# Kernel tuning notes

Hardware: AMD Instinct MI355X
Metric: run time of the kernel (lower is better)

The kernel has to match this reference:

```python
import jax, jax.numpy as jnp
import numpy as np

N = 50000
E = 400000
IN_DIM = 384
HID = 256
Q_DIM = 384
HEAD_HID = 128


def _glorot(key, shape):
    fan_in, fan_out = shape[0], shape[1]
    lim = float(np.sqrt(6.0 / (fan_in + fan_out)))
    return jax.random.uniform(key, shape, jnp.float32, -lim, lim)


def setup_inputs() -> dict:
    key = jax.random.key(0)
    ks = jax.random.split(key, 10)
    x = jax.random.normal(ks[0], (N, IN_DIM), jnp.float32)
    edge_index = jax.random.randint(ks[1], (2, E), 0, N, dtype=jnp.int64)
    q = jax.random.normal(ks[2], (Q_DIM,), jnp.float32)
    # layer 1: Linear(in_dim*2 + query_dim -> hidden)
    W1 = _glorot(ks[3], (IN_DIM * 2 + Q_DIM, HID))
    b1 = jnp.zeros((HID,), jnp.float32)
    # layer 2: Linear(hidden*2 + query_dim -> hidden)
    W2 = _glorot(ks[4], (HID * 2 + Q_DIM, HID))
    b2 = jnp.zeros((HID,), jnp.float32)
    # score head: Linear(hidden + query_dim -> 128) -> ReLU -> Linear(128 -> 1)
    Wh1 = _glorot(ks[5], (HID + Q_DIM, HEAD_HID))
    bh1 = jnp.zeros((HEAD_HID,), jnp.float32)
    Wh2 = _glorot(ks[6], (HEAD_HID, 1))
    bh2 = jnp.zeros((1,), jnp.float32)
    return {"x": x, "edge_index": edge_index, "q": q,
            "W1": W1, "b1": b1, "W2": W2, "b2": b2,
            "Wh1": Wh1, "bh1": bh1, "Wh2": Wh2, "bh2": bh2}


def _sage_layer(h, src, dst, q, W, b, n_nodes):
    # mean aggregation with self-loops: (sum_{j in N(i)} h_j + h_i) / (deg_i + 1)
    deg = jnp.zeros((n_nodes,), h.dtype).at[dst].add(1.0) + 1.0  # [N]
    agg = (jax.ops.segment_sum(h[src], dst, num_segments=n_nodes) + h) / deg[:, None]
    q_exp = jnp.broadcast_to(q, (n_nodes, q.shape[0]))
    cat = jnp.concatenate([h, agg, q_exp], axis=-1)  # [N, 2*d + q_dim]
    return jax.nn.relu(cat @ W + b)  # dropout is identity in eval mode


def reference(x, edge_index, q, W1, b1, W2, b2, Wh1, bh1, Wh2, bh2):
    src, dst = edge_index[0], edge_index[1]
    n = x.shape[0]
    h = _sage_layer(x, src, dst, q, W1, b1, n)
    h = _sage_layer(h, src, dst, q, W2, b2, n)
    q_exp = jnp.broadcast_to(q, (n, q.shape[0]))
    s = jax.nn.relu(jnp.concatenate([h, q_exp], axis=-1) @ Wh1 + bh1)
    logits = (s @ Wh2 + bh2).squeeze(-1)  # [N]
    return logits
```

## Files before the change

### kernel.cpp

```cpp
#include <hip/hip_runtime.h>
#include <cstdint>
#include <cstddef>

typedef unsigned short u16;
typedef short short8 __attribute__((ext_vector_type(8)));
typedef unsigned short u16x8 __attribute__((ext_vector_type(8)));
typedef unsigned short u16x4 __attribute__((ext_vector_type(4)));
typedef float f32x4 __attribute__((ext_vector_type(4)));

#define DEVI __device__ __forceinline__

#if defined(__has_builtin)
#if __has_builtin(__builtin_amdgcn_global_load_lds)
#define USE_GLD 1
#endif
#endif

DEVI float bf2f(u16 u) { return __uint_as_float(((unsigned)u) << 16); }
DEVI u16 f2bf(float f) {
  unsigned u = __float_as_uint(f);
  u += 0x7FFFu + ((u >> 16) & 1u);
  return (u16)(u >> 16);
}

DEVI void stage16(const u16* __restrict__ g, u16* lds_base, int lane) {
#ifdef USE_GLD
  __builtin_amdgcn_global_load_lds(
      (const __attribute__((address_space(1))) unsigned int*)g,
      (__attribute__((address_space(3))) unsigned int*)lds_base, 16, 0, 0);
#else
  *(u16x8*)(lds_base + lane * 8) = *(const u16x8*)g;
#endif
}

__global__ void build_deg(const int* __restrict__ dst, int* __restrict__ deg, int E) {
  int e = blockIdx.x * 256 + threadIdx.x;
  if (e < E) atomicAdd(&deg[dst[e]], 1);
}

__global__ __launch_bounds__(256) void scan1(const int* __restrict__ deg,
                                             int* __restrict__ pref,
                                             int* __restrict__ bsum, int Nn) {
  __shared__ int wsum[4];
  int i = blockIdx.x * 256 + threadIdx.x;
  int lane = threadIdx.x & 63, w = threadIdx.x >> 6;
  int v = (i < Nn) ? deg[i] : 0;
  int s = v;
  for (int off = 1; off < 64; off <<= 1) {
    int t = __shfl_up(s, off, 64);
    if (lane >= off) s += t;
  }
  if (lane == 63) wsum[w] = s;
  __syncthreads();
  int add = 0;
  for (int k = 0; k < w; ++k) add += wsum[k];
  int incl = s + add;
  if (i < Nn) pref[i] = incl - v;
  if (threadIdx.x == 255) bsum[blockIdx.x] = incl;
}

__global__ __launch_bounds__(256) void scan2(int* __restrict__ bsum,
                                             int* __restrict__ row_ofs,
                                             int nb, int Nn) {
  __shared__ int wsum[4];
  int t = threadIdx.x;
  int lane = t & 63, w = t >> 6;
  int v = (t < nb) ? bsum[t] : 0;
  int s = v;
  for (int off = 1; off < 64; off <<= 1) {
    int u = __shfl_up(s, off, 64);
    if (lane >= off) s += u;
  }
  if (lane == 63) wsum[w] = s;
  __syncthreads();
  int add = 0;
  for (int k = 0; k < w; ++k) add += wsum[k];
  int incl = s + add;
  if (t < nb) bsum[t] = incl - v;
  if (t == 255) row_ofs[Nn] = incl;
}

__global__ __launch_bounds__(256) void scan3(const int* __restrict__ pref,
                                             const int* __restrict__ bsum,
                                             int* __restrict__ row_ofs,
                                             int* __restrict__ cursor, int Nn) {
  int i = blockIdx.x * 256 + threadIdx.x;
  if (i < Nn) {
    int r = pref[i] + bsum[blockIdx.x];
    row_ofs[i] = r;
    cursor[i] = r;
  }
}

__global__ void csr_fill(const int* __restrict__ src, const int* __restrict__ dst,
                         int* __restrict__ cursor, int* __restrict__ col, int E) {
  int e = blockIdx.x * 256 + threadIdx.x;
  if (e < E) {
    int p = atomicAdd(&cursor[dst[e]], 1);
    col[p] = src[e];
  }
}

__global__ __launch_bounds__(256) void pack_all(
    const float* __restrict__ W1, const float* __restrict__ W2,
    const float* __restrict__ Wh1, u16* __restrict__ B1t,
    u16* __restrict__ B2t, u16* __restrict__ Bht) {
  int b = blockIdx.x;
  if (b < 1024) {
    int c = b >> 1;
    int k = (b & 1) * 256 + threadIdx.x;
    if (k < 384) {
      float v = (c < 256) ? W1[(size_t)k * 256 + c]
                          : W1[(size_t)(384 + k) * 256 + (c - 256)];
      B1t[(size_t)c * 384 + k] = f2bf(v);
    }
  } else if (b < 1536) {
    int c = b - 1024;
    int k = threadIdx.x;
    float v = (c < 256) ? W2[(size_t)k * 256 + c]
                        : W2[(size_t)(256 + k) * 256 + (c - 256)];
    B2t[(size_t)c * 256 + k] = f2bf(v);
  } else {
    int c = b - 1536;
    int k = threadIdx.x;
    Bht[(size_t)c * 256 + k] = f2bf(Wh1[(size_t)k * 128 + c]);
  }
}

__global__ __launch_bounds__(384) void bias_all(
    const float* __restrict__ W1, const float* __restrict__ b1,
    const float* __restrict__ W2, const float* __restrict__ b2,
    const float* __restrict__ Wh1, const float* __restrict__ bh1,
    const float* __restrict__ q, float* __restrict__ cq1,
    float* __restrict__ cq2, float* __restrict__ cqh) {
  __shared__ float part[6];
  int b = blockIdx.x;
  const float* W; const float* bb; float* o; int ld, roff, c;
  if (b < 256)      { W = W1;  bb = b1;  o = cq1; ld = 256; roff = 768; c = b; }
  else if (b < 512) { W = W2;  bb = b2;  o = cq2; ld = 256; roff = 512; c = b - 256; }
  else              { W = Wh1; bb = bh1; o = cqh; ld = 128; roff = 256; c = b - 512; }
  int t = threadIdx.x;
  float p = q[t] * W[(size_t)(roff + t) * ld + c];
  for (int off = 32; off > 0; off >>= 1) p += __shfl_down(p, off, 64);
  if ((t & 63) == 0) part[t >> 6] = p;
  __syncthreads();
  if (t == 0) {
    float acc = bb[c];
    for (int w = 0; w < 6; ++w) acc += part[w];
    o[c] = acc;
  }
}

#define W_NC 512
#define ES 520
#define OFF_A0 0
#define OFF_A1 (64 * 32)
#define OFF_B0 (2 * 64 * 32)
#define OFF_B1 (2 * 64 * 32 + 512 * 32)
#define SMEM_TOT (2 * 64 * 32 + 2 * 512 * 32)

#define GEMM512_COMPUTE(LA, LB)                                                \
  {                                                                            \
    short8 bfr[8];                                                             \
    _Pragma("unroll") for (int nt = 0; nt < 8; ++nt) bfr[nt] =                 \
        *(const short8*)&(LB)[((wave * 128 + nt * 16 + m) * 4 + csel) * 8];    \
    _Pragma("unroll") for (int mt = 0; mt < 4; ++mt) {                         \
      short8 af = *(const short8*)&(LA)[((mt * 16 + m) * 4 + csel) * 8];       \
      _Pragma("unroll") for (int nt = 0; nt < 8; ++nt)                         \
          acc[mt][nt] = __builtin_amdgcn_mfma_f32_16x16x32_bf16(               \
              af, bfr[nt], acc[mt][nt], 0, 0, 0);                              \
    }                                                                          \
  }

#define GEMM512_EPILOGUE()                                                     \
  {                                                                            \
    u16* et = lds_b0;                                                          \
    _Pragma("unroll") for (int mt = 0; mt < 4; ++mt) {                         \
      __syncthreads();                                                         \
      _Pragma("unroll") for (int nt = 0; nt < 8; ++nt) {                       \
        int col = wave * 128 + nt * 16 + m;                                    \
        float bb = (col < bias_len) ? bias[col] : 0.0f;                        \
        _Pragma("unroll") for (int r = 0; r < 4; ++r) {                        \
          float v = acc[mt][nt][r] + bb;                                       \
          if (relu) v = fmaxf(v, 0.0f);                                        \
          et[(quad * 4 + r) * ES + col] = f2bf(v);                             \
        }                                                                      \
      }                                                                        \
      __syncthreads();                                                         \
      _Pragma("unroll") for (int p = 0; p < 4; ++p) {                          \
        int row_loc = p * 4 + wave;                                            \
        int grow = row0 + mt * 16 + row_loc;                                   \
        if (grow < M)                                                          \
          *(u16x8*)&C[(size_t)grow * W_NC + lane * 8] =                        \
              *(const u16x8*)&et[row_loc * ES + lane * 8];                     \
      }                                                                        \
    }                                                                          \
  }

#define GEMM512_B_SETUP()                                                      \
  const u16* pbB[8];                                                           \
  _Pragma("unroll") for (int p = 0; p < 8; ++p) {                              \
    int L = p * 256 + tid;                                                     \
    int c = L >> 2, qs = L & 3;                                                \
    int g = qs ^ ((c >> 1) & 3);                                               \
    pbB[p] = Bt + (size_t)c * K + g * 8;                                       \
  }

#define GEMM512_B_STAGE2()                                                     \
  _Pragma("unroll") for (int p = 0; p < 8; ++p) {                              \
    u16* d = lds_b0 + (size_t)(p * 256 + wave * 64) * 8;                       \
    stage16(pbB[p], d, lane);                                                  \
    stage16(pbB[p] + 32, d + (512 * 32), lane);                                \
    pbB[p] += 64;                                                              \
  }

__global__ __launch_bounds__(256, 2) void gemm512_f32a(
    const float* __restrict__ A, const u16* __restrict__ Bt,
    u16* __restrict__ C, const float* __restrict__ bias,
    int M, int K, int bias_len, int relu) {
  __shared__ __align__(16) u16 smem[SMEM_TOT];
  u16* lds_a0 = smem + OFF_A0;
  u16* lds_a1 = smem + OFF_A1;
  u16* lds_b0 = smem + OFF_B0;
  u16* lds_b1 = smem + OFF_B1;

  const int tid = threadIdx.x;
  const int lane = tid & 63;
  const int wave = tid >> 6;
  const int row0 = blockIdx.x * 64;
  const int m = lane & 15;
  const int quad = lane >> 4;
  const int csel = quad ^ ((m >> 1) & 3);

  const int rA = tid >> 2;
  const int qA = tid & 3;
  const int sA = rA * 4 + (qA ^ ((rA >> 1) & 3));
  int ga = row0 + rA; if (ga >= M) ga = M - 1;
  const float* pa = A + (size_t)ga * K + qA * 8;

  GEMM512_B_SETUP()

  f32x4 acc[4][8] = {};

  f32x4 v0a = *(const f32x4*)pa, v0b = *(const f32x4*)(pa + 4);
  f32x4 v1a = *(const f32x4*)(pa + 32), v1b = *(const f32x4*)(pa + 36);
  pa += 64;

  for (int k0 = 0; k0 < K; k0 += 64) {
    __syncthreads();
    GEMM512_B_STAGE2()
    u16x8 h0, h1;
#pragma unroll
    for (int j = 0; j < 4; ++j) {
      h0[j] = f2bf(v0a[j]); h0[j + 4] = f2bf(v0b[j]);
      h1[j] = f2bf(v1a[j]); h1[j + 4] = f2bf(v1b[j]);
    }
    *(u16x8*)&lds_a0[sA * 8] = h0;
    *(u16x8*)&lds_a1[sA * 8] = h1;
    const float* pn = (k0 + 64 < K) ? pa : A;
    f32x4 n0a = *(const f32x4*)pn, n0b = *(const f32x4*)(pn + 4);
    f32x4 n1a = *(const f32x4*)(pn + 32), n1b = *(const f32x4*)(pn + 36);
    pa += 64;
    __syncthreads();
    GEMM512_COMPUTE(lds_a0, lds_b0)
    GEMM512_COMPUTE(lds_a1, lds_b1)
    v0a = n0a; v0b = n0b; v1a = n1a; v1b = n1b;
  }

  GEMM512_EPILOGUE()
}

__global__ __launch_bounds__(256, 2) void gemm512_bf16a(
    const u16* __restrict__ A, const u16* __restrict__ Bt,
    u16* __restrict__ C, const float* __restrict__ bias,
    int M, int K, int bias_len, int relu) {
  __shared__ __align__(16) u16 smem[SMEM_TOT];
  u16* lds_a0 = smem + OFF_A0;
  u16* lds_a1 = smem + OFF_A1;
  u16* lds_b0 = smem + OFF_B0;
  u16* lds_b1 = smem + OFF_B1;

  const int tid = threadIdx.x;
  const int lane = tid & 63;
  const int wave = tid >> 6;
  const int row0 = blockIdx.x * 64;
  const int m = lane & 15;
  const int quad = lane >> 4;
  const int csel = quad ^ ((m >> 1) & 3);

  const int rA = tid >> 2;
  const int qA = tid & 3;
  const int sA = rA * 4 + (qA ^ ((rA >> 1) & 3));
  int ga = row0 + rA; if (ga >= M) ga = M - 1;
  const u16* pa = A + (size_t)ga * K + qA * 8;

  GEMM512_B_SETUP()

  f32x4 acc[4][8] = {};

  u16x8 va0 = *(const u16x8*)pa;
  u16x8 va1 = *(const u16x8*)(pa + 32);
  pa += 64;

  for (int k0 = 0; k0 < K; k0 += 64) {
    __syncthreads();
    GEMM512_B_STAGE2()
    *(u16x8*)&lds_a0[sA * 8] = va0;
    *(u16x8*)&lds_a1[sA * 8] = va1;
    const u16* pn = (k0 + 64 < K) ? pa : A;
    u16x8 na0 = *(const u16x8*)pn;
    u16x8 na1 = *(const u16x8*)(pn + 32);
    pa += 64;
    __syncthreads();
    GEMM512_COMPUTE(lds_a0, lds_b0)
    GEMM512_COMPUTE(lds_a1, lds_b1)
    va0 = na0; va1 = na1;
  }

  GEMM512_EPILOGUE()
}

#define BM 128
#define BK 32

__global__ __launch_bounds__(256) void gemm_head(
    const u16* __restrict__ A, const u16* __restrict__ Bt,
    const float* __restrict__ cqh, const float* __restrict__ Wh2,
    const float* __restrict__ bh2, float* __restrict__ out, int M, int K) {
  __shared__ __align__(16) u16 lds_a[BM * BK];
  __shared__ __align__(16) u16 lds_b[BM * BK];
  __shared__ float red[128][2];

  const int tid = threadIdx.x;
  const int lane = tid & 63;
  const int wave = tid >> 6;
  const int wm = wave & 1, wn = wave >> 1;
  const int row0 = blockIdx.x * BM;
  const int m = lane & 15;
  const int quad = lane >> 4;
  const int csel = quad ^ ((m >> 1) & 3);

  const int r0 = tid >> 2, r1 = 64 + r0;
  const int cs = tid & 3;
  const int s0 = r0 * 4 + (cs ^ ((r0 >> 1) & 3));
  const int s1 = r1 * 4 + (cs ^ ((r1 >> 1) & 3));
  const int cb0 = cs ^ ((r0 >> 1) & 3);
  const int cb1 = cs ^ ((r1 >> 1) & 3);
  int ga0 = row0 + r0; if (ga0 >= M) ga0 = M - 1;
  int ga1 = row0 + r1; if (ga1 >= M) ga1 = M - 1;
  const u16* pa0 = A + (size_t)ga0 * K + cs * 8;
  const u16* pa1 = A + (size_t)ga1 * K + cs * 8;
  const u16* pb0 = Bt + (size_t)r0 * K + cb0 * 8;
  const u16* pb1 = Bt + (size_t)r1 * K + cb1 * 8;
  u16* lb0 = lds_b + (size_t)(wave * 64) * 8;
  u16* lb1 = lds_b + (size_t)(256 + wave * 64) * 8;

  f32x4 acc[4][4] = {};

  u16x8 va0 = *(const u16x8*)pa0; pa0 += BK;
  u16x8 va1 = *(const u16x8*)pa1; pa1 += BK;

  for (int k0 = 0; k0 < K; k0 += BK) {
    __syncthreads();
    stage16(pb0, lb0, lane); pb0 += BK;
    stage16(pb1, lb1, lane); pb1 += BK;
    *(u16x8*)&lds_a[s0 * 8] = va0;
    *(u16x8*)&lds_a[s1 * 8] = va1;
    const u16* n0 = (k0 + BK < K) ? pa0 : A;
    const u16* n1 = (k0 + BK < K) ? pa1 : A;
    u16x8 w0 = *(const u16x8*)n0;
    u16x8 w1 = *(const u16x8*)n1;
    pa0 += BK; pa1 += BK;
    __syncthreads();

    short8 af[4], bfv[4];
#pragma unroll
    for (int mt = 0; mt < 4; ++mt)
      af[mt] = *(const short8*)&lds_a[((wm * 64 + mt * 16 + m) * 4 + csel) * 8];
#pragma unroll
    for (int nt = 0; nt < 4; ++nt)
      bfv[nt] = *(const short8*)&lds_b[((wn * 64 + nt * 16 + m) * 4 + csel) * 8];
#pragma unroll
    for (int mt = 0; mt < 4; ++mt)
#pragma unroll
      for (int nt = 0; nt < 4; ++nt)
        acc[mt][nt] = __builtin_amdgcn_mfma_f32_16x16x32_bf16(
            af[mt], bfv[nt], acc[mt][nt], 0, 0, 0);
    va0 = w0; va1 = w1;
  }

  float part[4][4];
#pragma unroll
  for (int mt = 0; mt < 4; ++mt)
#pragma unroll
    for (int r = 0; r < 4; ++r) part[mt][r] = 0.0f;
#pragma unroll
  for (int nt = 0; nt < 4; ++nt) {
    int col = wn * 64 + nt * 16 + m;
    float bb = cqh[col];
    float w2 = Wh2[col];
#pragma unroll
    for (int mt = 0; mt < 4; ++mt)
#pragma unroll
      for (int r = 0; r < 4; ++r)
        part[mt][r] += fmaxf(acc[mt][nt][r] + bb, 0.0f) * w2;
  }
#pragma unroll
  for (int off = 8; off > 0; off >>= 1)
#pragma unroll
    for (int mt = 0; mt < 4; ++mt)
#pragma unroll
      for (int r = 0; r < 4; ++r)
        part[mt][r] += __shfl_xor(part[mt][r], off, 64);
  if (m == 0) {
#pragma unroll
    for (int mt = 0; mt < 4; ++mt)
#pragma unroll
      for (int r = 0; r < 4; ++r)
        red[wm * 64 + mt * 16 + quad * 4 + r][wn] = part[mt][r];
  }
  __syncthreads();
  if (tid < 128) {
    int grow = row0 + tid;
    if (grow < M) out[grow] = red[tid][0] + red[tid][1] + bh2[0];
  }
}

__global__ __launch_bounds__(256) void aggregate(
    const u16* __restrict__ C, const int* __restrict__ row_ofs,
    const int* __restrict__ col_idx, u16* __restrict__ H, int Nn) {
  int node = blockIdx.x * 8 + (threadIdx.x >> 5);
  if (node >= Nn) return;
  int l = threadIdx.x & 31;
  int s = row_ofs[node], e = row_ofs[node + 1];
  float inv = 1.0f / (float)(e - s + 1);
  const u16* crow = C + (size_t)node * 512;
  u16x8 y0 = *(const u16x8*)(crow + 256 + l * 8);
  float a[8];
#pragma unroll
  for (int j = 0; j < 8; ++j) a[j] = bf2f(y0[j]);
  int t = s;
  for (; t + 4 <= e; t += 4) {
    int j0 = col_idx[t], j1 = col_idx[t + 1], j2 = col_idx[t + 2], j3 = col_idx[t + 3];
    u16x8 v0 = *(const u16x8*)(C + (size_t)j0 * 512 + 256 + l * 8);
    u16x8 v1 = *(const u16x8*)(C + (size_t)j1 * 512 + 256 + l * 8);
    u16x8 v2 = *(const u16x8*)(C + (size_t)j2 * 512 + 256 + l * 8);
    u16x8 v3 = *(const u16x8*)(C + (size_t)j3 * 512 + 256 + l * 8);
#pragma unroll
    for (int j = 0; j < 8; ++j)
      a[j] += (bf2f(v0[j]) + bf2f(v1[j])) + (bf2f(v2[j]) + bf2f(v3[j]));
  }
  for (; t < e; ++t) {
    int jj = col_idx[t];
    u16x8 vj = *(const u16x8*)(C + (size_t)jj * 512 + 256 + l * 8);
#pragma unroll
    for (int j = 0; j < 8; ++j) a[j] += bf2f(vj[j]);
  }
  u16x8 u = *(const u16x8*)(crow + l * 8);
  u16x8 o;
#pragma unroll
  for (int j = 0; j < 8; ++j)
    o[j] = f2bf(fmaxf(bf2f(u[j]) + a[j] * inv, 0.0f));
  *(u16x8*)(H + (size_t)node * 256 + l * 8) = o;
}

extern "C" void kernel_launch(void* const* d_in, const int* in_sizes, int n_in,
                              void* d_out, int out_size, void* d_ws, size_t ws_size,
                              hipStream_t stream) {
  const float* x   = (const float*)d_in[0];
  const int*   ei  = (const int*)d_in[1];
  const float* q   = (const float*)d_in[2];
  const float* W1  = (const float*)d_in[3];
  const float* b1  = (const float*)d_in[4];
  const float* W2  = (const float*)d_in[5];
  const float* b2  = (const float*)d_in[6];
  const float* Wh1 = (const float*)d_in[7];
  const float* bh1 = (const float*)d_in[8];
  const float* Wh2 = (const float*)d_in[9];
  const float* bh2 = (const float*)d_in[10];

  const int N = in_sizes[0] / 384;
  const int E = in_sizes[1] / 2;
  const int Npad = ((N + 127) / 128) * 128;
  const int* esrc = ei;
  const int* edst = ei + E;

  size_t off = 0;
  auto alloc = [&](size_t bytes) -> void* {
    void* p = (char*)d_ws + off;
    off += (bytes + 255) & ~(size_t)255;
    return p;
  };
  int* deg     = (int*)alloc((size_t)N * 4);
  int* row_ofs = (int*)alloc((size_t)(N + 1) * 4);
  int* cursor  = (int*)alloc((size_t)N * 4);
  int* colidx  = (int*)alloc((size_t)E * 4);
  int* pref    = (int*)alloc((size_t)N * 4);
  int* bsum    = (int*)alloc(256 * 4);
  u16* B1t = (u16*)alloc((size_t)512 * 384 * 2);
  u16* B2t = (u16*)alloc((size_t)512 * 256 * 2);
  u16* Bht = (u16*)alloc((size_t)128 * 256 * 2);
  float* cq1 = (float*)alloc(256 * 4);
  float* cq2 = (float*)alloc(256 * 4);
  float* cqh = (float*)alloc(128 * 4);
  u16* Cbuf = (u16*)alloc((size_t)Npad * 512 * 2);
  u16* Hbuf = (u16*)alloc((size_t)Npad * 256 * 2);

  (void)hipMemsetAsync(deg, 0, (size_t)N * 4, stream);
  int eb = (E + 255) / 256;
  int nb = (N + 255) / 256;
  build_deg<<<eb, 256, 0, stream>>>(edst, deg, E);
  scan1<<<nb, 256, 0, stream>>>(deg, pref, bsum, N);
  scan2<<<1, 256, 0, stream>>>(bsum, row_ofs, nb, N);
  scan3<<<nb, 256, 0, stream>>>(pref, bsum, row_ofs, cursor, N);
  csr_fill<<<eb, 256, 0, stream>>>(esrc, edst, cursor, colidx, E);

  pack_all<<<1664, 256, 0, stream>>>(W1, W2, Wh1, B1t, B2t, Bht);
  bias_all<<<640, 384, 0, stream>>>(W1, b1, W2, b2, Wh1, bh1, q, cq1, cq2, cqh);

  int gb64 = (N + 63) / 64;
  int mb = Npad / 128;
  int nb8 = (N + 7) / 8;
  gemm512_f32a<<<gb64, 256, 0, stream>>>(x, B1t, Cbuf, cq1, N, 384, 256, 0);
  aggregate<<<nb8, 256, 0, stream>>>(Cbuf, row_ofs, colidx, Hbuf, N);
  gemm512_bf16a<<<gb64, 256, 0, stream>>>(Hbuf, B2t, Cbuf, cq2, N, 256, 256, 0);
  aggregate<<<nb8, 256, 0, stream>>>(Cbuf, row_ofs, colidx, Hbuf, N);
  gemm_head<<<mb, 256, 0, stream>>>(Hbuf, Bht, cqh, Wh2, bh2, (float*)d_out, N, 256);
}
```

Before: 339.6 us.

## Retile node GEMMs to 128x256 blocks with double-buffered LDS pipeline

Replaces the 64-row x 512-column GEMM blocks with 128-row x 256-column tiles, using 8 waves per block arranged 2x4, and splits the output columns across two blocks. The K loop now double-buffers A and B in LDS so that staging the next tile overlaps compute, leaving one barrier per iteration instead of two. This is meant to balance A/B reuse, cut accumulator registers per wave, and hide global-load latency. In exchange, the LDS footprint grows and the A tile is read twice, once per column half.

```diff
diff --git a/kernel.cpp b/kernel.cpp
--- a/kernel.cpp
+++ b/kernel.cpp
@@ -151,83 +151,87 @@
   }
 }
 
-#define W_NC 512
-#define ES 520
-#define OFF_A0 0
-#define OFF_A1 (64 * 32)
-#define OFF_B0 (2 * 64 * 32)
-#define OFF_B1 (2 * 64 * 32 + 512 * 32)
-#define SMEM_TOT (2 * 64 * 32 + 2 * 512 * 32)
-
-#define GEMM512_COMPUTE(LA, LB)                                                \
+#define G2_ACH 4096
+#define G2_ASZ 8192
+#define G2_BCH 8192
+#define G2_BSZ 16384
+#define G2_SMEM (2 * G2_ASZ + 2 * G2_BSZ)
+#define G2_ES 264
+
+#define G2_B_SETUP()                                                           \
+  const u16* pbB[2];                                                           \
+  _Pragma("unroll") for (int p = 0; p < 2; ++p) {                              \
+    int L = p * 512 + tid;                                                     \
+    int c = L >> 2, qs = L & 3;                                                \
+    int g = qs ^ ((c >> 1) & 3);                                               \
+    pbB[p] = Bt + (size_t)(cb * 256 + c) * K + g * 8;                          \
+  }
+
+#define G2_B_STAGE(LBDST)                                                      \
+  _Pragma("unroll") for (int p = 0; p < 2; ++p) {                              \
+    u16* d = (LBDST) + (size_t)(p * 512 + wave * 64) * 8;                      \
+    stage16(pbB[p], d, lane);                                                  \
+    stage16(pbB[p] + 32, d + G2_BCH, lane);                                    \
+    pbB[p] += 64;                                                              \
+  }
+
+#define G2_COMPUTE(LA, LB)                                                     \
+  _Pragma("unroll") for (int cc = 0; cc < 2; ++cc) {                           \
+    short8 bfr[4];                                                             \
+    _Pragma("unroll") for (int nt = 0; nt < 4; ++nt)                           \
+      bfr[nt] = *(const short8*)&(LB)[cc * G2_BCH +                            \
+                  ((wc * 64 + nt * 16 + m) * 4 + csel) * 8];                   \
+    _Pragma("unroll") for (int mt = 0; mt < 4; ++mt) {                         \
+      short8 af = *(const short8*)&(LA)[cc * G2_ACH +                          \
+                  ((wr * 64 + mt * 16 + m) * 4 + csel) * 8];                   \
+      _Pragma("unroll") for (int nt = 0; nt < 4; ++nt)                         \
+        acc[mt][nt] = __builtin_amdgcn_mfma_f32_16x16x32_bf16(                 \
+            af, bfr[nt], acc[mt][nt], 0, 0, 0);                                \
+    }                                                                          \
+  }
+
+#define G2_EPILOGUE()                                                          \
   {                                                                            \
-    short8 bfr[8];                                                             \
-    _Pragma("unroll") for (int nt = 0; nt < 8; ++nt) bfr[nt] =                 \
-        *(const short8*)&(LB)[((wave * 128 + nt * 16 + m) * 4 + csel) * 8];    \
-    _Pragma("unroll") for (int mt = 0; mt < 4; ++mt) {                         \
-      short8 af = *(const short8*)&(LA)[((mt * 16 + m) * 4 + csel) * 8];       \
-      _Pragma("unroll") for (int nt = 0; nt < 8; ++nt)                         \
-          acc[mt][nt] = __builtin_amdgcn_mfma_f32_16x16x32_bf16(               \
-              af, bfr[nt], acc[mt][nt], 0, 0, 0);                              \
-    }                                                                          \
-  }
-
-#define GEMM512_EPILOGUE()                                                     \
-  {                                                                            \
-    u16* et = lds_b0;                                                          \
-    _Pragma("unroll") for (int mt = 0; mt < 4; ++mt) {                         \
-      __syncthreads();                                                         \
-      _Pragma("unroll") for (int nt = 0; nt < 8; ++nt) {                       \
-        int col = wave * 128 + nt * 16 + m;                                    \
-        float bb = (col < bias_len) ? bias[col] : 0.0f;                        \
-        _Pragma("unroll") for (int r = 0; r < 4; ++r) {                        \
-          float v = acc[mt][nt][r] + bb;                                       \
-          if (relu) v = fmaxf(v, 0.0f);                                        \
-          et[(quad * 4 + r) * ES + col] = f2bf(v);                             \
-        }                                                                      \
-      }                                                                        \
-      __syncthreads();                                                         \
-      _Pragma("unroll") for (int p = 0; p < 4; ++p) {                          \
-        int row_loc = p * 4 + wave;                                            \
-        int grow = row0 + mt * 16 + row_loc;                                   \
-        if (grow < M)                                                          \
-          *(u16x8*)&C[(size_t)grow * W_NC + lane * 8] =                        \
-              *(const u16x8*)&et[row_loc * ES + lane * 8];                     \
+    u16* et = smem;                                                            \
+    _Pragma("unroll") for (int mt = 0; mt < 4; ++mt)                           \
+    _Pragma("unroll") for (int nt = 0; nt < 4; ++nt) {                         \
+      int colL = wc * 64 + nt * 16 + m;                                        \
+      int gcol = cb * 256 + colL;                                              \
+      float bb = (gcol < bias_len) ? bias[gcol] : 0.0f;                        \
+      _Pragma("unroll") for (int r = 0; r < 4; ++r) {                          \
+        float v = acc[mt][nt][r] + bb;                                         \
+        if (relu) v = fmaxf(v, 0.0f);                                          \
+        et[(wr * 64 + mt * 16 + quad * 4 + r) * G2_ES + colL] = f2bf(v);       \
       }                                                                        \
     }                                                                          \
-  }
-
-#define GEMM512_B_SETUP()                                                      \
-  const u16* pbB[8];                                                           \
-  _Pragma("unroll") for (int p = 0; p < 8; ++p) {                              \
-    int L = p * 256 + tid;                                                     \
-    int c = L >> 2, qs = L & 3;                                                \
-    int g = qs ^ ((c >> 1) & 3);                                               \
-    pbB[p] = Bt + (size_t)c * K + g * 8;                                       \
-  }
-
-#define GEMM512_B_STAGE2()                                                     \
-  _Pragma("unroll") for (int p = 0; p < 8; ++p) {                              \
-    u16* d = lds_b0 + (size_t)(p * 256 + wave * 64) * 8;                       \
-    stage16(pbB[p], d, lane);                                                  \
-    stage16(pbB[p] + 32, d + (512 * 32), lane);                                \
-    pbB[p] += 64;                                                              \
-  }
-
-__global__ __launch_bounds__(256, 2) void gemm512_f32a(
+    __syncthreads();                                                           \
+    _Pragma("unroll") for (int rep = 0; rep < 8; ++rep) {                      \
+      int idx = rep * 512 + tid;                                               \
+      int row = idx >> 5, ch = idx & 31;                                       \
+      int grow = row0 + row;                                                   \
+      if (grow < M)                                                            \
+        *(u16x8*)&C[(size_t)grow * 512 + cb * 256 + ch * 8] =                  \
+            *(const u16x8*)&et[row * G2_ES + ch * 8];                          \
+    }                                                                          \
+  }
+
+__global__ __launch_bounds__(512, 2) void gemm256_f32a(
     const float* __restrict__ A, const u16* __restrict__ Bt,
     u16* __restrict__ C, const float* __restrict__ bias,
     int M, int K, int bias_len, int relu) {
-  __shared__ __align__(16) u16 smem[SMEM_TOT];
-  u16* lds_a0 = smem + OFF_A0;
-  u16* lds_a1 = smem + OFF_A1;
-  u16* lds_b0 = smem + OFF_B0;
-  u16* lds_b1 = smem + OFF_B1;
+  __shared__ __align__(16) u16 smem[G2_SMEM];
+  u16* a0 = smem;
+  u16* a1 = smem + G2_ASZ;
+  u16* b0 = smem + 2 * G2_ASZ;
+  u16* b1 = b0 + G2_BSZ;
 
   const int tid = threadIdx.x;
   const int lane = tid & 63;
   const int wave = tid >> 6;
-  const int row0 = blockIdx.x * 64;
+  const int wr = wave >> 2;
+  const int wc = wave & 3;
+  const int cb = blockIdx.x & 1;
+  const int row0 = (blockIdx.x >> 1) * 128;
   const int m = lane & 15;
   const int quad = lane >> 4;
   const int csel = quad ^ ((m >> 1) & 3);
@@ -238,52 +242,78 @@
   int ga = row0 + rA; if (ga >= M) ga = M - 1;
   const float* pa = A + (size_t)ga * K + qA * 8;
 
-  GEMM512_B_SETUP()
-
-  f32x4 acc[4][8] = {};
+  G2_B_SETUP()
+
+  f32x4 acc[4][4] = {};
 
   f32x4 v0a = *(const f32x4*)pa, v0b = *(const f32x4*)(pa + 4);
   f32x4 v1a = *(const f32x4*)(pa + 32), v1b = *(const f32x4*)(pa + 36);
   pa += 64;
 
-  for (int k0 = 0; k0 < K; k0 += 64) {
-    __syncthreads();
-    GEMM512_B_STAGE2()
+  G2_B_STAGE(b0)
+  {
     u16x8 h0, h1;
 #pragma unroll
     for (int j = 0; j < 4; ++j) {
       h0[j] = f2bf(v0a[j]); h0[j + 4] = f2bf(v0b[j]);
       h1[j] = f2bf(v1a[j]); h1[j + 4] = f2bf(v1b[j]);
     }
-    *(u16x8*)&lds_a0[sA * 8] = h0;
-    *(u16x8*)&lds_a1[sA * 8] = h1;
-    const float* pn = (k0 + 64 < K) ? pa : A;
-    f32x4 n0a = *(const f32x4*)pn, n0b = *(const f32x4*)(pn + 4);
-    f32x4 n1a = *(const f32x4*)(pn + 32), n1b = *(const f32x4*)(pn + 36);
+    *(u16x8*)&a0[sA * 8] = h0;
+    *(u16x8*)&a0[G2_ACH + sA * 8] = h1;
+  }
+  {
+    const float* pn = (64 < K) ? pa : A;
+    v0a = *(const f32x4*)pn; v0b = *(const f32x4*)(pn + 4);
+    v1a = *(const f32x4*)(pn + 32); v1b = *(const f32x4*)(pn + 36);
     pa += 64;
+  }
+  __syncthreads();
+
+  const int NT = K >> 6;
+  for (int t = 0; t < NT; ++t) {
+    u16* la  = (t & 1) ? a1 : a0;
+    u16* lb  = (t & 1) ? b1 : b0;
+    u16* lan = (t & 1) ? a0 : a1;
+    u16* lbn = (t & 1) ? b0 : b1;
+    if (t + 1 < NT) {
+      G2_B_STAGE(lbn)
+      u16x8 h0, h1;
+#pragma unroll
+      for (int j = 0; j < 4; ++j) {
+        h0[j] = f2bf(v0a[j]); h0[j + 4] = f2bf(v0b[j]);
+        h1[j] = f2bf(v1a[j]); h1[j + 4] = f2bf(v1b[j]);
+      }
+      *(u16x8*)&lan[sA * 8] = h0;
+      *(u16x8*)&lan[G2_ACH + sA * 8] = h1;
+      const float* pn = (t + 2 < NT) ? pa : A;
+      v0a = *(const f32x4*)pn; v0b = *(const f32x4*)(pn + 4);
+      v1a = *(const f32x4*)(pn + 32); v1b = *(const f32x4*)(pn + 36);
+      pa += 64;
+    }
+    G2_COMPUTE(la, lb)
     __syncthreads();
-    GEMM512_COMPUTE(lds_a0, lds_b0)
-    GEMM512_COMPUTE(lds_a1, lds_b1)
-    v0a = n0a; v0b = n0b; v1a = n1a; v1b = n1b;
-  }
-
-  GEMM512_EPILOGUE()
-}
-
-__global__ __launch_bounds__(256, 2) void gemm512_bf16a(
+  }
+
+  G2_EPILOGUE()
+}
+
+__global__ __launch_bounds__(512, 2) void gemm256_bf16a(
     const u16* __restrict__ A, const u16* __restrict__ Bt,
     u16* __restrict__ C, const float* __restrict__ bias,
     int M, int K, int bias_len, int relu) {
-  __shared__ __align__(16) u16 smem[SMEM_TOT];
-  u16* lds_a0 = smem + OFF_A0;
-  u16* lds_a1 = smem + OFF_A1;
-  u16* lds_b0 = smem + OFF_B0;
-  u16* lds_b1 = smem + OFF_B1;
+  __shared__ __align__(16) u16 smem[G2_SMEM];
+  u16* a0 = smem;
+  u16* a1 = smem + G2_ASZ;
+  u16* b0 = smem + 2 * G2_ASZ;
+  u16* b1 = b0 + G2_BSZ;
 
   const int tid = threadIdx.x;
   const int lane = tid & 63;
   const int wave = tid >> 6;
-  const int row0 = blockIdx.x * 64;
+  const int wr = wave >> 2;
+  const int wc = wave & 3;
+  const int cb = blockIdx.x & 1;
+  const int row0 = (blockIdx.x >> 1) * 128;
   const int m = lane & 15;
   const int quad = lane >> 4;
   const int csel = quad ^ ((m >> 1) & 3);
@@ -294,30 +324,45 @@
   int ga = row0 + rA; if (ga >= M) ga = M - 1;
   const u16* pa = A + (size_t)ga * K + qA * 8;
 
-  GEMM512_B_SETUP()
-
-  f32x4 acc[4][8] = {};
+  G2_B_SETUP()
+
+  f32x4 acc[4][4] = {};
 
   u16x8 va0 = *(const u16x8*)pa;
   u16x8 va1 = *(const u16x8*)(pa + 32);
   pa += 64;
 
-  for (int k0 = 0; k0 < K; k0 += 64) {
+  G2_B_STAGE(b0)
+  *(u16x8*)&a0[sA * 8] = va0;
+  *(u16x8*)&a0[G2_ACH + sA * 8] = va1;
+  {
+    const u16* pn = (64 < K) ? pa : A;
+    va0 = *(const u16x8*)pn;
+    va1 = *(const u16x8*)(pn + 32);
+    pa += 64;
+  }
+  __syncthreads();
+
+  const int NT = K >> 6;
+  for (int t = 0; t < NT; ++t) {
+    u16* la  = (t & 1) ? a1 : a0;
+    u16* lb  = (t & 1) ? b1 : b0;
+    u16* lan = (t & 1) ? a0 : a1;
+    u16* lbn = (t & 1) ? b0 : b1;
+    if (t + 1 < NT) {
+      G2_B_STAGE(lbn)
+      *(u16x8*)&lan[sA * 8] = va0;
+      *(u16x8*)&lan[G2_ACH + sA * 8] = va1;
+      const u16* pn = (t + 2 < NT) ? pa : A;
+      va0 = *(const u16x8*)pn;
+      va1 = *(const u16x8*)(pn + 32);
+      pa += 64;
+    }
+    G2_COMPUTE(la, lb)
     __syncthreads();
-    GEMM512_B_STAGE2()
-    *(u16x8*)&lds_a0[sA * 8] = va0;
-    *(u16x8*)&lds_a1[sA * 8] = va1;
-    const u16* pn = (k0 + 64 < K) ? pa : A;
-    u16x8 na0 = *(const u16x8*)pn;
-    u16x8 na1 = *(const u16x8*)(pn + 32);
-    pa += 64;
-    __syncthreads();
-    GEMM512_COMPUTE(lds_a0, lds_b0)
-    GEMM512_COMPUTE(lds_a1, lds_b1)
-    va0 = na0; va1 = na1;
-  }
-
-  GEMM512_EPILOGUE()
+  }
+
+  G2_EPILOGUE()
 }
 
 #define BM 128
@@ -518,12 +563,12 @@
   pack_all<<<1664, 256, 0, stream>>>(W1, W2, Wh1, B1t, B2t, Bht);
   bias_all<<<640, 384, 0, stream>>>(W1, b1, W2, b2, Wh1, bh1, q, cq1, cq2, cqh);
 
-  int gb64 = (N + 63) / 64;
+  int gb2 = ((N + 127) / 128) * 2;
   int mb = Npad / 128;
   int nb8 = (N + 7) / 8;
-  gemm512_f32a<<<gb64, 256, 0, stream>>>(x, B1t, Cbuf, cq1, N, 384, 256, 0);
+  gemm256_f32a<<<gb2, 512, 0, stream>>>(x, B1t, Cbuf, cq1, N, 384, 256, 0);
   aggregate<<<nb8, 256, 0, stream>>>(Cbuf, row_ofs, colidx, Hbuf, N);
-  gemm512_bf16a<<<gb64, 256, 0, stream>>>(Hbuf, B2t, Cbuf, cq2, N, 256, 256, 0);
+  gemm256_bf16a<<<gb2, 512, 0, stream>>>(Hbuf, B2t, Cbuf, cq2, N, 256, 256, 0);
   aggregate<<<nb8, 256, 0, stream>>>(Cbuf, row_ofs, colidx, Hbuf, N);
   gemm_head<<<mb, 256, 0, stream>>>(Hbuf, Bht, cqh, Wh2, bh2, (float*)d_out, N, 256);
 }
```

After: 350.0 us. 1.03x slower.

## Double-buffer GEMM LDS tiles with one barrier per K-step of 32

Applied to the files above, without the earlier changes.

The two 512-column GEMM kernels used to stage a 64-wide K chunk into LDS and then compute it, with two __syncthreads per iteration. They now ping-pong between two LDS buffers per 32-wide K step: the next tile's B (global_load_lds) and A are issued before computing the current one. A single s_waitcnt plus s_barrier per step replaces the two syncs. This is meant to overlap global-to-LDS transfers with MFMA work, at the cost of more loop iterations and reliance on hand-written vmcnt counts.

```diff
diff --git a/kernel.cpp b/kernel.cpp
--- a/kernel.cpp
+++ b/kernel.cpp
@@ -153,28 +153,45 @@
 
 #define W_NC 512
 #define ES 520
-#define OFF_A0 0
-#define OFF_A1 (64 * 32)
-#define OFF_B0 (2 * 64 * 32)
-#define OFF_B1 (2 * 64 * 32 + 512 * 32)
-#define SMEM_TOT (2 * 64 * 32 + 2 * 512 * 32)
-
-#define GEMM512_COMPUTE(LA, LB)                                                \
+#define V2_ASZ 2048
+#define V2_BSZ 16384
+#define V2_SMEM (2 * V2_ASZ + 2 * V2_BSZ)
+
+#define V2_BARRIER(vm)                                                         \
+  asm volatile("s_waitcnt vmcnt(" #vm ") lgkmcnt(0)\n\ts_barrier" ::: "memory");
+
+#define V2_B_SETUP()                                                           \
+  const u16* pbB[8];                                                           \
+  _Pragma("unroll") for (int p = 0; p < 8; ++p) {                              \
+    int L = p * 256 + tid;                                                     \
+    int c = L >> 2, qs = L & 3;                                                \
+    int g = qs ^ ((c >> 1) & 3);                                               \
+    pbB[p] = Bt + (size_t)c * K + g * 8;                                       \
+  }
+
+#define V2_B_STAGE(DST)                                                        \
+  _Pragma("unroll") for (int p = 0; p < 8; ++p) {                              \
+    stage16(pbB[p], (DST) + (size_t)(p * 256 + wave * 64) * 8, lane);          \
+    pbB[p] += 32;                                                              \
+  }
+
+#define V2_COMPUTE(LA, LB)                                                     \
   {                                                                            \
     short8 bfr[8];                                                             \
-    _Pragma("unroll") for (int nt = 0; nt < 8; ++nt) bfr[nt] =                 \
-        *(const short8*)&(LB)[((wave * 128 + nt * 16 + m) * 4 + csel) * 8];    \
+    _Pragma("unroll") for (int nt = 0; nt < 8; ++nt)                           \
+      bfr[nt] =                                                                \
+          *(const short8*)&(LB)[((wave * 128 + nt * 16 + m) * 4 + csel) * 8];  \
     _Pragma("unroll") for (int mt = 0; mt < 4; ++mt) {                         \
       short8 af = *(const short8*)&(LA)[((mt * 16 + m) * 4 + csel) * 8];       \
       _Pragma("unroll") for (int nt = 0; nt < 8; ++nt)                         \
-          acc[mt][nt] = __builtin_amdgcn_mfma_f32_16x16x32_bf16(               \
-              af, bfr[nt], acc[mt][nt], 0, 0, 0);                              \
+        acc[mt][nt] = __builtin_amdgcn_mfma_f32_16x16x32_bf16(                 \
+            af, bfr[nt], acc[mt][nt], 0, 0, 0);                                \
     }                                                                          \
   }
 
-#define GEMM512_EPILOGUE()                                                     \
+#define V2_EPILOGUE()                                                          \
   {                                                                            \
-    u16* et = lds_b0;                                                          \
+    u16* et = smem + 2 * V2_ASZ;                                               \
     _Pragma("unroll") for (int mt = 0; mt < 4; ++mt) {                         \
       __syncthreads();                                                         \
       _Pragma("unroll") for (int nt = 0; nt < 8; ++nt) {                       \
@@ -197,32 +214,15 @@
     }                                                                          \
   }
 
-#define GEMM512_B_SETUP()                                                      \
-  const u16* pbB[8];                                                           \
-  _Pragma("unroll") for (int p = 0; p < 8; ++p) {                              \
-    int L = p * 256 + tid;                                                     \
-    int c = L >> 2, qs = L & 3;                                                \
-    int g = qs ^ ((c >> 1) & 3);                                               \
-    pbB[p] = Bt + (size_t)c * K + g * 8;                                       \
-  }
-
-#define GEMM512_B_STAGE2()                                                     \
-  _Pragma("unroll") for (int p = 0; p < 8; ++p) {                              \
-    u16* d = lds_b0 + (size_t)(p * 256 + wave * 64) * 8;                       \
-    stage16(pbB[p], d, lane);                                                  \
-    stage16(pbB[p] + 32, d + (512 * 32), lane);                                \
-    pbB[p] += 64;                                                              \
-  }
-
-__global__ __launch_bounds__(256, 2) void gemm512_f32a(
+__global__ __launch_bounds__(256, 2) void gemm512v2_f32a(
     const float* __restrict__ A, const u16* __restrict__ Bt,
     u16* __restrict__ C, const float* __restrict__ bias,
     int M, int K, int bias_len, int relu) {
-  __shared__ __align__(16) u16 smem[SMEM_TOT];
-  u16* lds_a0 = smem + OFF_A0;
-  u16* lds_a1 = smem + OFF_A1;
-  u16* lds_b0 = smem + OFF_B0;
-  u16* lds_b1 = smem + OFF_B1;
+  __shared__ __align__(16) u16 smem[V2_SMEM];
+  u16* a0 = smem;
+  u16* a1 = smem + V2_ASZ;
+  u16* b0 = smem + 2 * V2_ASZ;
+  u16* b1 = b0 + V2_BSZ;
 
   const int tid = threadIdx.x;
   const int lane = tid & 63;
@@ -238,47 +238,58 @@
   int ga = row0 + rA; if (ga >= M) ga = M - 1;
   const float* pa = A + (size_t)ga * K + qA * 8;
 
-  GEMM512_B_SETUP()
+  V2_B_SETUP()
 
   f32x4 acc[4][8] = {};
 
-  f32x4 v0a = *(const f32x4*)pa, v0b = *(const f32x4*)(pa + 4);
-  f32x4 v1a = *(const f32x4*)(pa + 32), v1b = *(const f32x4*)(pa + 36);
-  pa += 64;
-
-  for (int k0 = 0; k0 < K; k0 += 64) {
-    __syncthreads();
-    GEMM512_B_STAGE2()
-    u16x8 h0, h1;
-#pragma unroll
-    for (int j = 0; j < 4; ++j) {
-      h0[j] = f2bf(v0a[j]); h0[j + 4] = f2bf(v0b[j]);
-      h1[j] = f2bf(v1a[j]); h1[j + 4] = f2bf(v1b[j]);
+  f32x4 vlo = *(const f32x4*)pa, vhi = *(const f32x4*)(pa + 4);
+  pa += 32;
+  V2_B_STAGE(b0)
+  {
+    u16x8 h;
+#pragma unroll
+    for (int j = 0; j < 4; ++j) { h[j] = f2bf(vlo[j]); h[j + 4] = f2bf(vhi[j]); }
+    *(u16x8*)&a0[sA * 8] = h;
+  }
+  {
+    const float* pn = (32 < K) ? pa : A;
+    vlo = *(const f32x4*)pn; vhi = *(const f32x4*)(pn + 4);
+    pa += 32;
+  }
+  V2_BARRIER(2)
+
+  const int NT = K >> 5;
+  for (int t = 0; t < NT; ++t) {
+    u16* la  = (t & 1) ? a1 : a0;
+    u16* lb  = (t & 1) ? b1 : b0;
+    u16* lan = (t & 1) ? a0 : a1;
+    u16* lbn = (t & 1) ? b0 : b1;
+    if (t + 1 < NT) {
+      V2_B_STAGE(lbn)
+      u16x8 h;
+#pragma unroll
+      for (int j = 0; j < 4; ++j) { h[j] = f2bf(vlo[j]); h[j + 4] = f2bf(vhi[j]); }
+      *(u16x8*)&lan[sA * 8] = h;
+      const float* pn = (t + 2 < NT) ? pa : A;
+      vlo = *(const f32x4*)pn; vhi = *(const f32x4*)(pn + 4);
+      pa += 32;
     }
-    *(u16x8*)&lds_a0[sA * 8] = h0;
-    *(u16x8*)&lds_a1[sA * 8] = h1;
-    const float* pn = (k0 + 64 < K) ? pa : A;
-    f32x4 n0a = *(const f32x4*)pn, n0b = *(const f32x4*)(pn + 4);
-    f32x4 n1a = *(const f32x4*)(pn + 32), n1b = *(const f32x4*)(pn + 36);
-    pa += 64;
-    __syncthreads();
-    GEMM512_COMPUTE(lds_a0, lds_b0)
-    GEMM512_COMPUTE(lds_a1, lds_b1)
-    v0a = n0a; v0b = n0b; v1a = n1a; v1b = n1b;
-  }
-
-  GEMM512_EPILOGUE()
-}
-
-__global__ __launch_bounds__(256, 2) void gemm512_bf16a(
+    V2_COMPUTE(la, lb)
+    V2_BARRIER(2)
+  }
+
+  V2_EPILOGUE()
+}
+
+__global__ __launch_bounds__(256, 2) void gemm512v2_bf16a(
     const u16* __restrict__ A, const u16* __restrict__ Bt,
     u16* __restrict__ C, const float* __restrict__ bias,
     int M, int K, int bias_len, int relu) {
-  __shared__ __align__(16) u16 smem[SMEM_TOT];
-  u16* lds_a0 = smem + OFF_A0;
-  u16* lds_a1 = smem + OFF_A1;
-  u16* lds_b0 = smem + OFF_B0;
-  u16* lds_b1 = smem + OFF_B1;
+  __shared__ __align__(16) u16 smem[V2_SMEM];
+  u16* a0 = smem;
+  u16* a1 = smem + V2_ASZ;
+  u16* b0 = smem + 2 * V2_ASZ;
+  u16* b1 = b0 + V2_BSZ;
 
   const int tid = threadIdx.x;
   const int lane = tid & 63;
@@ -294,30 +305,39 @@
   int ga = row0 + rA; if (ga >= M) ga = M - 1;
   const u16* pa = A + (size_t)ga * K + qA * 8;
 
-  GEMM512_B_SETUP()
+  V2_B_SETUP()
 
   f32x4 acc[4][8] = {};
 
-  u16x8 va0 = *(const u16x8*)pa;
-  u16x8 va1 = *(const u16x8*)(pa + 32);
-  pa += 64;
-
-  for (int k0 = 0; k0 < K; k0 += 64) {
-    __syncthreads();
-    GEMM512_B_STAGE2()
-    *(u16x8*)&lds_a0[sA * 8] = va0;
-    *(u16x8*)&lds_a1[sA * 8] = va1;
-    const u16* pn = (k0 + 64 < K) ? pa : A;
-    u16x8 na0 = *(const u16x8*)pn;
-    u16x8 na1 = *(const u16x8*)(pn + 32);
-    pa += 64;
-    __syncthreads();
-    GEMM512_COMPUTE(lds_a0, lds_b0)
-    GEMM512_COMPUTE(lds_a1, lds_b1)
-    va0 = na0; va1 = na1;
-  }
-
-  GEMM512_EPILOGUE()
+  u16x8 va = *(const u16x8*)pa;
+  pa += 32;
+  V2_B_STAGE(b0)
+  *(u16x8*)&a0[sA * 8] = va;
+  {
+    const u16* pn = (32 < K) ? pa : A;
+    va = *(const u16x8*)pn;
+    pa += 32;
+  }
+  V2_BARRIER(1)
+
+  const int NT = K >> 5;
+  for (int t = 0; t < NT; ++t) {
+    u16* la  = (t & 1) ? a1 : a0;
+    u16* lb  = (t & 1) ? b1 : b0;
+    u16* lan = (t & 1) ? a0 : a1;
+    u16* lbn = (t & 1) ? b0 : b1;
+    if (t + 1 < NT) {
+      V2_B_STAGE(lbn)
+      *(u16x8*)&lan[sA * 8] = va;
+      const u16* pn = (t + 2 < NT) ? pa : A;
+      va = *(const u16x8*)pn;
+      pa += 32;
+    }
+    V2_COMPUTE(la, lb)
+    V2_BARRIER(1)
+  }
+
+  V2_EPILOGUE()
 }
 
 #define BM 128
@@ -521,9 +541,9 @@
   int gb64 = (N + 63) / 64;
   int mb = Npad / 128;
   int nb8 = (N + 7) / 8;
-  gemm512_f32a<<<gb64, 256, 0, stream>>>(x, B1t, Cbuf, cq1, N, 384, 256, 0);
+  gemm512v2_f32a<<<gb64, 256, 0, stream>>>(x, B1t, Cbuf, cq1, N, 384, 256, 0);
   aggregate<<<nb8, 256, 0, stream>>>(Cbuf, row_ofs, colidx, Hbuf, N);
-  gemm512_bf16a<<<gb64, 256, 0, stream>>>(Hbuf, B2t, Cbuf, cq2, N, 256, 256, 0);
+  gemm512v2_bf16a<<<gb64, 256, 0, stream>>>(Hbuf, B2t, Cbuf, cq2, N, 256, 256, 0);
   aggregate<<<nb8, 256, 0, stream>>>(Cbuf, row_ofs, colidx, Hbuf, N);
   gemm_head<<<mb, 256, 0, stream>>>(Hbuf, Bht, cqh, Wh2, bh2, (float*)d_out, N, 256);
 }
```

Result: slower. 348.2 us (+2.5%).

## Widen GEMM blocks to 128 rows with 8 waves sharing staged weight tile

Applied to the files above, without the earlier changes.

The two node GEMMs now use 512-thread blocks covering 128 rows instead of 64. Eight waves are arranged 2x4 (wr, wc), so each staged 512-column weight tile in LDS is reused by twice as many rows. This halves the per-row global and LDS traffic for loading the weight matrix. The cost is a larger block with higher LDS use (about 80KB), which may limit occupancy. The epilogue is reworked to write 32 rows per mt step.

```diff
diff --git a/kernel.cpp b/kernel.cpp
--- a/kernel.cpp
+++ b/kernel.cpp
@@ -153,81 +153,84 @@
 
 #define W_NC 512
 #define ES 520
-#define OFF_A0 0
-#define OFF_A1 (64 * 32)
-#define OFF_B0 (2 * 64 * 32)
-#define OFF_B1 (2 * 64 * 32 + 512 * 32)
-#define SMEM_TOT (2 * 64 * 32 + 2 * 512 * 32)
-
-#define GEMM512_COMPUTE(LA, LB)                                                \
+#define V3_ACH 4096
+#define V3_BCH 16384
+#define V3_SMEM (2 * V3_ACH + 2 * V3_BCH)
+
+#define V3_B_SETUP()                                                           \
+  const u16* pbB[4];                                                           \
+  _Pragma("unroll") for (int p = 0; p < 4; ++p) {                              \
+    int L = p * 512 + tid;                                                     \
+    int c = L >> 2, qs = L & 3;                                                \
+    int g = qs ^ ((c >> 1) & 3);                                               \
+    pbB[p] = Bt + (size_t)c * K + g * 8;                                       \
+  }
+
+#define V3_B_STAGE2()                                                          \
+  _Pragma("unroll") for (int p = 0; p < 4; ++p) {                              \
+    u16* d = lds_b0 + (size_t)(p * 512 + wave * 64) * 8;                       \
+    stage16(pbB[p], d, lane);                                                  \
+    stage16(pbB[p] + 32, d + V3_BCH, lane);                                    \
+    pbB[p] += 64;                                                              \
+  }
+
+#define V3_COMPUTE(LA, LB)                                                     \
   {                                                                            \
     short8 bfr[8];                                                             \
-    _Pragma("unroll") for (int nt = 0; nt < 8; ++nt) bfr[nt] =                 \
-        *(const short8*)&(LB)[((wave * 128 + nt * 16 + m) * 4 + csel) * 8];    \
+    _Pragma("unroll") for (int nt = 0; nt < 8; ++nt)                           \
+      bfr[nt] =                                                                \
+          *(const short8*)&(LB)[((wc * 128 + nt * 16 + m) * 4 + csel) * 8];    \
     _Pragma("unroll") for (int mt = 0; mt < 4; ++mt) {                         \
-      short8 af = *(const short8*)&(LA)[((mt * 16 + m) * 4 + csel) * 8];       \
+      short8 af =                                                              \
+          *(const short8*)&(LA)[((wr * 64 + mt * 16 + m) * 4 + csel) * 8];     \
       _Pragma("unroll") for (int nt = 0; nt < 8; ++nt)                         \
-          acc[mt][nt] = __builtin_amdgcn_mfma_f32_16x16x32_bf16(               \
-              af, bfr[nt], acc[mt][nt], 0, 0, 0);                              \
+        acc[mt][nt] = __builtin_amdgcn_mfma_f32_16x16x32_bf16(                 \
+            af, bfr[nt], acc[mt][nt], 0, 0, 0);                                \
     }                                                                          \
   }
 
-#define GEMM512_EPILOGUE()                                                     \
+#define V3_EPILOGUE()                                                          \
   {                                                                            \
-    u16* et = lds_b0;                                                          \
+    u16* et = smem;                                                            \
     _Pragma("unroll") for (int mt = 0; mt < 4; ++mt) {                         \
       __syncthreads();                                                         \
       _Pragma("unroll") for (int nt = 0; nt < 8; ++nt) {                       \
-        int col = wave * 128 + nt * 16 + m;                                    \
+        int col = wc * 128 + nt * 16 + m;                                      \
         float bb = (col < bias_len) ? bias[col] : 0.0f;                        \
         _Pragma("unroll") for (int r = 0; r < 4; ++r) {                        \
           float v = acc[mt][nt][r] + bb;                                       \
           if (relu) v = fmaxf(v, 0.0f);                                        \
-          et[(quad * 4 + r) * ES + col] = f2bf(v);                             \
+          et[(wr * 16 + quad * 4 + r) * ES + col] = f2bf(v);                   \
         }                                                                      \
       }                                                                        \
       __syncthreads();                                                         \
-      _Pragma("unroll") for (int p = 0; p < 4; ++p) {                          \
-        int row_loc = p * 4 + wave;                                            \
-        int grow = row0 + mt * 16 + row_loc;                                   \
+      _Pragma("unroll") for (int rep = 0; rep < 4; ++rep) {                    \
+        int idx = rep * 512 + tid;                                             \
+        int row = idx >> 6, ch = idx & 63;                                     \
+        int grow = row0 + (row >> 4) * 64 + mt * 16 + (row & 15);              \
         if (grow < M)                                                          \
-          *(u16x8*)&C[(size_t)grow * W_NC + lane * 8] =                        \
-              *(const u16x8*)&et[row_loc * ES + lane * 8];                     \
+          *(u16x8*)&C[(size_t)grow * W_NC + ch * 8] =                          \
+              *(const u16x8*)&et[row * ES + ch * 8];                           \
       }                                                                        \
     }                                                                          \
   }
 
-#define GEMM512_B_SETUP()                                                      \
-  const u16* pbB[8];                                                           \
-  _Pragma("unroll") for (int p = 0; p < 8; ++p) {                              \
-    int L = p * 256 + tid;                                                     \
-    int c = L >> 2, qs = L & 3;                                                \
-    int g = qs ^ ((c >> 1) & 3);                                               \
-    pbB[p] = Bt + (size_t)c * K + g * 8;                                       \
-  }
-
-#define GEMM512_B_STAGE2()                                                     \
-  _Pragma("unroll") for (int p = 0; p < 8; ++p) {                              \
-    u16* d = lds_b0 + (size_t)(p * 256 + wave * 64) * 8;                       \
-    stage16(pbB[p], d, lane);                                                  \
-    stage16(pbB[p] + 32, d + (512 * 32), lane);                                \
-    pbB[p] += 64;                                                              \
-  }
-
-__global__ __launch_bounds__(256, 2) void gemm512_f32a(
+__global__ __launch_bounds__(512, 2) void gemm512w_f32a(
     const float* __restrict__ A, const u16* __restrict__ Bt,
     u16* __restrict__ C, const float* __restrict__ bias,
     int M, int K, int bias_len, int relu) {
-  __shared__ __align__(16) u16 smem[SMEM_TOT];
-  u16* lds_a0 = smem + OFF_A0;
-  u16* lds_a1 = smem + OFF_A1;
-  u16* lds_b0 = smem + OFF_B0;
-  u16* lds_b1 = smem + OFF_B1;
+  __shared__ __align__(16) u16 smem[V3_SMEM];
+  u16* lds_a0 = smem;
+  u16* lds_a1 = smem + V3_ACH;
+  u16* lds_b0 = smem + 2 * V3_ACH;
+  u16* lds_b1 = lds_b0 + V3_BCH;
 
   const int tid = threadIdx.x;
   const int lane = tid & 63;
   const int wave = tid >> 6;
-  const int row0 = blockIdx.x * 64;
+  const int wr = wave >> 2;
+  const int wc = wave & 3;
+  const int row0 = blockIdx.x * 128;
   const int m = lane & 15;
   const int quad = lane >> 4;
   const int csel = quad ^ ((m >> 1) & 3);
@@ -238,7 +241,7 @@
   int ga = row0 + rA; if (ga >= M) ga = M - 1;
   const float* pa = A + (size_t)ga * K + qA * 8;
 
-  GEMM512_B_SETUP()
+  V3_B_SETUP()
 
   f32x4 acc[4][8] = {};
 
@@ -248,7 +251,7 @@
 
   for (int k0 = 0; k0 < K; k0 += 64) {
     __syncthreads();
-    GEMM512_B_STAGE2()
+    V3_B_STAGE2()
     u16x8 h0, h1;
 #pragma unroll
     for (int j = 0; j < 4; ++j) {
@@ -262,28 +265,30 @@
     f32x4 n1a = *(const f32x4*)(pn + 32), n1b = *(const f32x4*)(pn + 36);
     pa += 64;
     __syncthreads();
-    GEMM512_COMPUTE(lds_a0, lds_b0)
-    GEMM512_COMPUTE(lds_a1, lds_b1)
+    V3_COMPUTE(lds_a0, lds_b0)
+    V3_COMPUTE(lds_a1, lds_b1)
     v0a = n0a; v0b = n0b; v1a = n1a; v1b = n1b;
   }
 
-  GEMM512_EPILOGUE()
-}
-
-__global__ __launch_bounds__(256, 2) void gemm512_bf16a(
+  V3_EPILOGUE()
+}
+
+__global__ __launch_bounds__(512, 2) void gemm512w_bf16a(
     const u16* __restrict__ A, const u16* __restrict__ Bt,
     u16* __restrict__ C, const float* __restrict__ bias,
     int M, int K, int bias_len, int relu) {
-  __shared__ __align__(16) u16 smem[SMEM_TOT];
-  u16* lds_a0 = smem + OFF_A0;
-  u16* lds_a1 = smem + OFF_A1;
-  u16* lds_b0 = smem + OFF_B0;
-  u16* lds_b1 = smem + OFF_B1;
+  __shared__ __align__(16) u16 smem[V3_SMEM];
+  u16* lds_a0 = smem;
+  u16* lds_a1 = smem + V3_ACH;
+  u16* lds_b0 = smem + 2 * V3_ACH;
+  u16* lds_b1 = lds_b0 + V3_BCH;
 
   const int tid = threadIdx.x;
   const int lane = tid & 63;
   const int wave = tid >> 6;
-  const int row0 = blockIdx.x * 64;
+  const int wr = wave >> 2;
+  const int wc = wave & 3;
+  const int row0 = blockIdx.x * 128;
   const int m = lane & 15;
   const int quad = lane >> 4;
   const int csel = quad ^ ((m >> 1) & 3);
@@ -294,7 +299,7 @@
   int ga = row0 + rA; if (ga >= M) ga = M - 1;
   const u16* pa = A + (size_t)ga * K + qA * 8;
 
-  GEMM512_B_SETUP()
+  V3_B_SETUP()
 
   f32x4 acc[4][8] = {};
 
@@ -304,7 +309,7 @@
 
   for (int k0 = 0; k0 < K; k0 += 64) {
     __syncthreads();
-    GEMM512_B_STAGE2()
+    V3_B_STAGE2()
     *(u16x8*)&lds_a0[sA * 8] = va0;
     *(u16x8*)&lds_a1[sA * 8] = va1;
     const u16* pn = (k0 + 64 < K) ? pa : A;
@@ -312,12 +317,12 @@
     u16x8 na1 = *(const u16x8*)(pn + 32);
     pa += 64;
     __syncthreads();
-    GEMM512_COMPUTE(lds_a0, lds_b0)
-    GEMM512_COMPUTE(lds_a1, lds_b1)
+    V3_COMPUTE(lds_a0, lds_b0)
+    V3_COMPUTE(lds_a1, lds_b1)
     va0 = na0; va1 = na1;
   }
 
-  GEMM512_EPILOGUE()
+  V3_EPILOGUE()
 }
 
 #define BM 128
@@ -518,12 +523,12 @@
   pack_all<<<1664, 256, 0, stream>>>(W1, W2, Wh1, B1t, B2t, Bht);
   bias_all<<<640, 384, 0, stream>>>(W1, b1, W2, b2, Wh1, bh1, q, cq1, cq2, cqh);
 
-  int gb64 = (N + 63) / 64;
+  int gb128 = (N + 127) / 128;
   int mb = Npad / 128;
   int nb8 = (N + 7) / 8;
-  gemm512_f32a<<<gb64, 256, 0, stream>>>(x, B1t, Cbuf, cq1, N, 384, 256, 0);
+  gemm512w_f32a<<<gb128, 512, 0, stream>>>(x, B1t, Cbuf, cq1, N, 384, 256, 0);
   aggregate<<<nb8, 256, 0, stream>>>(Cbuf, row_ofs, colidx, Hbuf, N);
-  gemm512_bf16a<<<gb64, 256, 0, stream>>>(Hbuf, B2t, Cbuf, cq2, N, 256, 256, 0);
+  gemm512w_bf16a<<<gb128, 512, 0, stream>>>(Hbuf, B2t, Cbuf, cq2, N, 256, 256, 0);
   aggregate<<<nb8, 256, 0, stream>>>(Cbuf, row_ofs, colidx, Hbuf, N);
   gemm_head<<<mb, 256, 0, stream>>>(Hbuf, Bht, cqh, Wh2, bh2, (float*)d_out, N, 256);
 }
```

After: 343.7 us. Within noise of the previous version (+1.2%).
